# Performance work log

Hardware: AMD Instinct MI355X
Metric: run time of the kernel (lower is better)

## Reference

```python
import jax, jax.numpy as jnp
import numpy as np

N, F_IN, F_OUT = 8192, 512, 128
NEG_SLOPE = 0.2
MASK_VAL = -9e16


def setup_inputs() -> dict:
    key = jax.random.key(0)
    k_x, k_adj, k_w, k_a = jax.random.split(key, 4)
    x = jax.random.normal(k_x, (N, F_IN), dtype=jnp.float32)
    adj = jax.random.randint(k_adj, (N, N), 0, 2, dtype=jnp.int32)
    # xavier_normal_ init: std = sqrt(2 / (fan_in + fan_out))
    w = jax.random.normal(k_w, (F_IN, F_OUT), dtype=jnp.float32) * np.sqrt(2.0 / (F_IN + F_OUT))
    a = jax.random.normal(k_a, (2 * F_OUT, 1), dtype=jnp.float32) * np.sqrt(2.0 / (2 * F_OUT + 1))
    return {"x": x, "adj": adj, "w": w, "a": a}


def reference(x, adj, w, a):
    f_out = w.shape[1]
    h = x @ w                                   # [N, f_out]
    source_scores = h @ a[:f_out]               # [N, 1]
    target_scores = h @ a[f_out:]               # [N, 1]
    e = source_scores + target_scores.T         # [N, N] outer sum
    e = jax.nn.leaky_relu(e, negative_slope=NEG_SLOPE)
    e = jnp.where(adj > 0, e, jnp.float32(MASK_VAL))
    attention = jax.nn.softmax(e, axis=-1)      # [N, N]
    h_prime = attention @ h                     # [N, f_out]
    return attention, h_prime
```

## Files before the change

### kernel.cpp

```cpp
#include <hip/hip_runtime.h>
#include <hip/hip_bf16.h>

typedef unsigned short u16;
typedef unsigned int u32;
typedef __attribute__((ext_vector_type(8))) short short8;
typedef __attribute__((ext_vector_type(4))) float f32x4;

#define NN 8192
#define FIN 512
#define FOUT 128
#define NEG 0.2f
#define L2E 1.44269504088896340736f
#define EXP2(x) __builtin_amdgcn_exp2f(x)
#define LOG2(x) __builtin_amdgcn_logf(x)

__device__ __forceinline__ u16 f2bf(float f) {
  u32 u = __builtin_bit_cast(u32, f);
  u32 r = (u + 0x7fffu + ((u >> 16) & 1u)) >> 16;
  return (u16)r;
}

__global__ __launch_bounds__(256) void k_h(const float* __restrict__ x,
                                           const float* __restrict__ w,
                                           const float* __restrict__ av,
                                           u16* __restrict__ hb,
                                           float* __restrict__ sg,
                                           float* __restrict__ tgo) {
  __shared__ float xs[16][68];
  __shared__ float ws_[64][128];
  __shared__ u16 ht[16][130];
  const int t = threadIdx.x;
  const int r0 = blockIdx.x * 16;
  const int r = t >> 4;
  const int cq = (t & 15) * 4;
  float acc[2][4] = {};
  for (int kc = 0; kc < FIN; kc += 64) {
    __syncthreads();
    {
      const int rr = t >> 4, cc = (t & 15) * 4;
      *(float4*)&xs[rr][cc] = *(const float4*)(x + (size_t)(r0 + rr) * FIN + kc + cc);
    }
#pragma unroll
    for (int i = 0; i < 8; ++i) {
      const int off = i * 1024 + t * 4;
      const int wr = off >> 7, wc = off & 127;
      *(float4*)&ws_[wr][wc] = *(const float4*)(w + (size_t)(kc + wr) * FOUT + wc);
    }
    __syncthreads();
    for (int kk = 0; kk < 64; ++kk) {
      const float xv = xs[r][kk];
#pragma unroll
      for (int g = 0; g < 2; ++g) {
        const float4 wv = *(const float4*)&ws_[kk][cq + 64 * g];
        acc[g][0] = fmaf(xv, wv.x, acc[g][0]);
        acc[g][1] = fmaf(xv, wv.y, acc[g][1]);
        acc[g][2] = fmaf(xv, wv.z, acc[g][2]);
        acc[g][3] = fmaf(xv, wv.w, acc[g][3]);
      }
    }
  }
  const int rg = r0 + r;
  float sp = 0.f, tp = 0.f;
#pragma unroll
  for (int g = 0; g < 2; ++g) {
#pragma unroll
    for (int e = 0; e < 4; ++e) {
      const int n = cq + 64 * g + e;
      const float v = acc[g][e];
      ht[r][n] = f2bf(v);
      sp = fmaf(v, av[n], sp);
      tp = fmaf(v, av[FOUT + n], tp);
    }
  }
#pragma unroll
  for (int d = 1; d < 16; d <<= 1) {
    sp += __shfl_xor(sp, d);
    tp += __shfl_xor(tp, d);
  }
  if ((t & 15) == 0) { sg[rg] = sp; tgo[rg] = tp; }
  __syncthreads();
  {
    const int half = blockIdx.x & 1;
    u16* dst = hb + (size_t)(blockIdx.x >> 1) * 4096;
    union { short8 v; u16 us[8]; } b1;
    const int i1 = t * 8;
    const int o1 = (i1 >> 8) * 512 + half * 256 + (i1 & 255);
    const int nblk = i1 >> 8;
#pragma unroll
    for (int q = 0; q < 8; ++q) {
      const int j = (i1 + q) & 255;
      b1.us[q] = ht[((j >> 7) & 1) * 8 + (j & 7)][nblk * 16 + ((j >> 3) & 15)];
    }
    *(short8*)(dst + o1) = b1.v;
  }
}

__global__ __launch_bounds__(1024, 2) void k_maskA(const int* __restrict__ adj,
                                                   const float* __restrict__ sg,
                                                   const float* __restrict__ tg,
                                                   u32* __restrict__ maskR,
                                                   u32* __restrict__ maskT,
                                                   float* __restrict__ c2g) {
  __shared__ u32 mlds[16][257];
  const int tid = threadIdx.x;
  const int w = tid >> 6, lane = tid & 63;
  const int r0 = blockIdx.x << 4;
  const int row = r0 + w;
  const float sv = sg[row];
  const int4* ap = (const int4*)(adj + (size_t)row * NN);
  float sum = 0.f;
#pragma unroll 4
  for (int it = 0; it < 32; ++it) {
    const int4 a0 = ap[it * 64 + lane];
    const float4 tv = *(const float4*)(tg + it * 256 + lane * 4);
    u32 nib = 0u;
    float e, p, sm = 0.f;
    e = sv + tv.x; e = fmaxf(e, NEG * e); p = EXP2(e * L2E); sm += (a0.x > 0) ? p : 0.f; nib |= (a0.x > 0) ? 1u : 0u;
    e = sv + tv.y; e = fmaxf(e, NEG * e); p = EXP2(e * L2E); sm += (a0.y > 0) ? p : 0.f; nib |= (a0.y > 0) ? 2u : 0u;
    e = sv + tv.z; e = fmaxf(e, NEG * e); p = EXP2(e * L2E); sm += (a0.z > 0) ? p : 0.f; nib |= (a0.z > 0) ? 4u : 0u;
    e = sv + tv.w; e = fmaxf(e, NEG * e); p = EXP2(e * L2E); sm += (a0.w > 0) ? p : 0.f; nib |= (a0.w > 0) ? 8u : 0u;
    sum += sm;
    u32 v0 = nib;
    v0 |= __shfl_xor(v0, 1) << 4;
    v0 |= __shfl_xor(v0, 2) << 8;
    v0 |= __shfl_xor(v0, 4) << 16;
    if ((lane & 7) == 0) mlds[w][it * 8 + (lane >> 3)] = v0;
  }
#pragma unroll
  for (int d = 1; d < 64; d <<= 1) sum += __shfl_xor(sum, d);
  if (lane == 0) c2g[row] = -LOG2(sum);
  __syncthreads();
  for (int idx = tid; idx < 4096; idx += 1024) {
    const u32 v = mlds[idx >> 8][idx & 255];
    maskR[(size_t)(r0 + (idx >> 8)) * 256 + (idx & 255)] = v;
    maskT[(size_t)(idx & 255) * NN + r0 + (idx >> 8)] = v;
  }
}

__global__ __launch_bounds__(512, 4) void k_spv(const float* __restrict__ sg,
                                                const float* __restrict__ tg,
                                                const float* __restrict__ c2g,
                                                const u32* __restrict__ maskR,
                                                const u32* __restrict__ maskT,
                                                const u16* __restrict__ hb,
                                                float* __restrict__ att,
                                                float* __restrict__ part) {
  const int tid = threadIdx.x;
  const int w = tid >> 6, lane = tid & 63;
  if (blockIdx.x < 512) {
    const int mt = blockIdx.x >> 3, kt = blockIdx.x & 7;
    const int wr = w >> 1, ch = w & 1;
    const int wrow = mt * 128 + wr * 32;
    const int arow = lane & 15, kg = lane >> 4;
    const int rowA = wrow + arow, rowB = wrow + 16 + arow;
    const float sA = sg[rowA], cA = c2g[rowA];
    const float sB = sg[rowB], cB = c2g[rowB];
    f32x4 acc0[4], acc1[4];
#pragma unroll
    for (int j = 0; j < 4; ++j) {
      acc0[j] = (f32x4){0.f, 0.f, 0.f, 0.f};
      acc1[j] = (f32x4){0.f, 0.f, 0.f, 0.f};
    }
    const int kg8 = kg * 8;
#pragma unroll 2
    for (int step = 0; step < 32; ++step) {
      const int kgrp = kt * 32 + step;
      const int k0 = kgrp * 32;
      const u32 wdA = maskT[(size_t)kgrp * NN + rowA];
      const u32 wdB = maskT[(size_t)kgrp * NN + rowB];
      const u32 bA = (wdA >> kg8) & 0xffu;
      const u32 bB = (wdB >> kg8) & 0xffu;
      const float4 t0 = *(const float4*)(tg + k0 + kg8);
      const float4 t1 = *(const float4*)(tg + k0 + kg8 + 4);
      const float tv[8] = {t0.x, t0.y, t0.z, t0.w, t1.x, t1.y, t1.z, t1.w};
      union { short8 s8; u32 u[4]; } afA, afB;
      {
        float p[8];
#pragma unroll
        for (int e = 0; e < 8; ++e) {
          float ev = sA + tv[e];
          ev = fmaxf(ev, NEG * ev);
          p[e] = ((bA >> e) & 1u) ? EXP2(fmaf(ev, L2E, cA)) : 0.f;
        }
#pragma unroll
        for (int h2 = 0; h2 < 4; ++h2)
          afA.u[h2] = (u32)f2bf(p[2 * h2]) | ((u32)f2bf(p[2 * h2 + 1]) << 16);
      }
      {
        float p[8];
#pragma unroll
        for (int e = 0; e < 8; ++e) {
          float ev = sB + tv[e];
          ev = fmaxf(ev, NEG * ev);
          p[e] = ((bB >> e) & 1u) ? EXP2(fmaf(ev, L2E, cB)) : 0.f;
        }
#pragma unroll
        for (int h2 = 0; h2 < 4; ++h2)
          afB.u[h2] = (u32)f2bf(p[2 * h2]) | ((u32)f2bf(p[2 * h2 + 1]) << 16);
      }
      const u16* base = hb + (size_t)kgrp * 4096 + ch * 2048 + lane * 8;
#pragma unroll
      for (int j = 0; j < 4; ++j) {
        const short8 bf = *(const short8*)(base + j * 512);
        acc0[j] = __builtin_amdgcn_mfma_f32_16x16x32_bf16(afA.s8, bf, acc0[j], 0, 0, 0);
        acc1[j] = __builtin_amdgcn_mfma_f32_16x16x32_bf16(afB.s8, bf, acc1[j], 0, 0, 0);
      }
    }
    float* pslice = part + (size_t)kt * (NN * FOUT);
#pragma unroll
    for (int j = 0; j < 4; ++j) {
      const int col = (ch * 4 + j) * 16 + arow;
#pragma unroll
      for (int q = 0; q < 4; ++q) {
        pslice[(size_t)(wrow + kg * 4 + q) * FOUT + col] = acc0[j][q];
        pslice[(size_t)(wrow + 16 + kg * 4 + q) * FOUT + col] = acc1[j][q];
      }
    }
  } else {
    const int sb = blockIdx.x - 512;
    const int row = sb * 4 + (w >> 1);
    const int half = w & 1;
    const float sv = sg[row];
    const float c2 = c2g[row];
    const u32* mrow = maskR + (size_t)row * 256 + half * 128;
    const float* tbase = tg + half * 4096;
    float* abase = att + (size_t)row * NN + half * 4096;
    const u32 sh = (lane & 7) * 4;
#pragma unroll 4
    for (int it = 0; it < 16; ++it) {
      const int jo = it * 256 + lane * 4;
      const u32 wd = mrow[it * 8 + (lane >> 3)];
      const u32 nib = (wd >> sh) & 0xfu;
      const float4 tv = *(const float4*)(tbase + jo);
      float e0 = sv + tv.x; e0 = fmaxf(e0, NEG * e0);
      float e1 = sv + tv.y; e1 = fmaxf(e1, NEG * e1);
      float e2 = sv + tv.z; e2 = fmaxf(e2, NEG * e2);
      float e3 = sv + tv.w; e3 = fmaxf(e3, NEG * e3);
      f32x4 o;
      o.x = (nib & 1u) ? EXP2(fmaf(e0, L2E, c2)) : 0.f;
      o.y = (nib & 2u) ? EXP2(fmaf(e1, L2E, c2)) : 0.f;
      o.z = (nib & 4u) ? EXP2(fmaf(e2, L2E, c2)) : 0.f;
      o.w = (nib & 8u) ? EXP2(fmaf(e3, L2E, c2)) : 0.f;
      __builtin_nontemporal_store(o, (f32x4*)(abase + jo));
    }
  }
}

__global__ __launch_bounds__(256) void k_red(const float* __restrict__ part,
                                             float* __restrict__ hp) {
  const int i = (blockIdx.x * 256 + threadIdx.x) * 4;
  f32x4 s = (f32x4){0.f, 0.f, 0.f, 0.f};
#pragma unroll
  for (int kt = 0; kt < 8; ++kt)
    s += *(const f32x4*)(part + (size_t)kt * (NN * FOUT) + i);
  *(f32x4*)(hp + i) = s;
}

extern "C" void kernel_launch(void* const* d_in, const int* in_sizes, int n_in,
                              void* d_out, int out_size, void* d_ws, size_t ws_size,
                              hipStream_t stream) {
  const float* x = (const float*)d_in[0];
  const int* adj = (const int*)d_in[1];
  const float* w = (const float*)d_in[2];
  const float* a = (const float*)d_in[3];
  float* out = (float*)d_out;
  float* att = out;
  float* hp = out + (size_t)NN * NN;
  u16* hb = (u16*)d_ws;
  float* s = (float*)((char*)d_ws + (size_t)2 * 1024 * 1024);
  float* t = s + NN;
  float* c2 = t + NN;
  u32* maskR = (u32*)((char*)d_ws + (size_t)4 * 1024 * 1024);
  u32* maskT = (u32*)((char*)d_ws + (size_t)12 * 1024 * 1024);
  float* part = (float*)((char*)d_ws + (size_t)20 * 1024 * 1024);

  k_h<<<512, 256, 0, stream>>>(x, w, a, hb, s, t);
  k_maskA<<<512, 1024, 0, stream>>>(adj, s, t, maskR, maskT, c2);
  k_spv<<<2560, 512, 0, stream>>>(s, t, c2, maskR, maskT, hb, att, part);
  k_red<<<1024, 256, 0, stream>>>(part, hp);
}
```

Measured before the change: 188.5 us.

## Fuse attention-row write into mask pass; split PV matmul into own kernel

The mask/row-sum kernel now keeps each row's mask bits in registers and writes the normalized attention row immediately after computing the log-sum. This removes the row-major mask buffer and the separate attention-writing blocks in the combined kernel. The transposed mask is written directly to global memory without an LDS staging step, and adj is read with nontemporal loads. The PV matmul becomes its own smaller launch. In exchange, the exponentials are recomputed in the same kernel, which lengthens it, and the transposed-mask stores become scattered 4-byte writes.

```diff
diff --git a/kernel.cpp b/kernel.cpp
--- a/kernel.cpp
+++ b/kernel.cpp
@@ -5,6 +5,7 @@
 typedef unsigned int u32;
 typedef __attribute__((ext_vector_type(8))) short short8;
 typedef __attribute__((ext_vector_type(4))) float f32x4;
+typedef __attribute__((ext_vector_type(4))) int i32x4;
 
 #define NN 8192
 #define FIN 512
@@ -95,23 +96,21 @@
   }
 }
 
-__global__ __launch_bounds__(1024, 2) void k_maskA(const int* __restrict__ adj,
-                                                   const float* __restrict__ sg,
-                                                   const float* __restrict__ tg,
-                                                   u32* __restrict__ maskR,
-                                                   u32* __restrict__ maskT,
-                                                   float* __restrict__ c2g) {
-  __shared__ u32 mlds[16][257];
-  const int tid = threadIdx.x;
-  const int w = tid >> 6, lane = tid & 63;
-  const int r0 = blockIdx.x << 4;
-  const int row = r0 + w;
+__global__ __launch_bounds__(512, 2) void k_fms(const int* __restrict__ adj,
+                                                const float* __restrict__ sg,
+                                                const float* __restrict__ tg,
+                                                u32* __restrict__ maskT,
+                                                float* __restrict__ c2g,
+                                                float* __restrict__ att) {
+  const int w = threadIdx.x >> 6, lane = threadIdx.x & 63;
+  const int row = blockIdx.x * 8 + w;
   const float sv = sg[row];
-  const int4* ap = (const int4*)(adj + (size_t)row * NN);
+  const i32x4* ap = (const i32x4*)(adj + (size_t)row * NN);
+  u32 bank[4] = {0u, 0u, 0u, 0u};
   float sum = 0.f;
-#pragma unroll 4
+#pragma unroll
   for (int it = 0; it < 32; ++it) {
-    const int4 a0 = ap[it * 64 + lane];
+    const i32x4 a0 = __builtin_nontemporal_load(ap + it * 64 + lane);
     const float4 tv = *(const float4*)(tg + it * 256 + lane * 4);
     u32 nib = 0u;
     float e, p, sm = 0.f;
@@ -120,128 +119,110 @@
     e = sv + tv.z; e = fmaxf(e, NEG * e); p = EXP2(e * L2E); sm += (a0.z > 0) ? p : 0.f; nib |= (a0.z > 0) ? 4u : 0u;
     e = sv + tv.w; e = fmaxf(e, NEG * e); p = EXP2(e * L2E); sm += (a0.w > 0) ? p : 0.f; nib |= (a0.w > 0) ? 8u : 0u;
     sum += sm;
+    bank[it >> 3] |= nib << ((it & 7) * 4);
     u32 v0 = nib;
     v0 |= __shfl_xor(v0, 1) << 4;
     v0 |= __shfl_xor(v0, 2) << 8;
     v0 |= __shfl_xor(v0, 4) << 16;
-    if ((lane & 7) == 0) mlds[w][it * 8 + (lane >> 3)] = v0;
+    if ((lane & 7) == 0)
+      maskT[(size_t)(it * 8 + (lane >> 3)) * NN + row] = v0;
   }
 #pragma unroll
   for (int d = 1; d < 64; d <<= 1) sum += __shfl_xor(sum, d);
-  if (lane == 0) c2g[row] = -LOG2(sum);
-  __syncthreads();
-  for (int idx = tid; idx < 4096; idx += 1024) {
-    const u32 v = mlds[idx >> 8][idx & 255];
-    maskR[(size_t)(r0 + (idx >> 8)) * 256 + (idx & 255)] = v;
-    maskT[(size_t)(idx & 255) * NN + r0 + (idx >> 8)] = v;
-  }
-}
-
-__global__ __launch_bounds__(512, 4) void k_spv(const float* __restrict__ sg,
-                                                const float* __restrict__ tg,
-                                                const float* __restrict__ c2g,
-                                                const u32* __restrict__ maskR,
-                                                const u32* __restrict__ maskT,
-                                                const u16* __restrict__ hb,
-                                                float* __restrict__ att,
-                                                float* __restrict__ part) {
+  const float c2 = -LOG2(sum);
+  if (lane == 0) c2g[row] = c2;
+  float* abase = att + (size_t)row * NN;
+#pragma unroll
+  for (int it = 0; it < 32; ++it) {
+    const u32 nib = (bank[it >> 3] >> ((it & 7) * 4)) & 0xfu;
+    const float4 tv = *(const float4*)(tg + it * 256 + lane * 4);
+    float e0 = sv + tv.x; e0 = fmaxf(e0, NEG * e0);
+    float e1 = sv + tv.y; e1 = fmaxf(e1, NEG * e1);
+    float e2 = sv + tv.z; e2 = fmaxf(e2, NEG * e2);
+    float e3 = sv + tv.w; e3 = fmaxf(e3, NEG * e3);
+    f32x4 o;
+    o.x = (nib & 1u) ? EXP2(fmaf(e0, L2E, c2)) : 0.f;
+    o.y = (nib & 2u) ? EXP2(fmaf(e1, L2E, c2)) : 0.f;
+    o.z = (nib & 4u) ? EXP2(fmaf(e2, L2E, c2)) : 0.f;
+    o.w = (nib & 8u) ? EXP2(fmaf(e3, L2E, c2)) : 0.f;
+    __builtin_nontemporal_store(o, (f32x4*)(abase + it * 256 + lane * 4));
+  }
+}
+
+__global__ __launch_bounds__(512, 2) void k_pv(const float* __restrict__ sg,
+                                               const float* __restrict__ tg,
+                                               const float* __restrict__ c2g,
+                                               const u32* __restrict__ maskT,
+                                               const u16* __restrict__ hb,
+                                               float* __restrict__ part) {
   const int tid = threadIdx.x;
   const int w = tid >> 6, lane = tid & 63;
-  if (blockIdx.x < 512) {
-    const int mt = blockIdx.x >> 3, kt = blockIdx.x & 7;
-    const int wr = w >> 1, ch = w & 1;
-    const int wrow = mt * 128 + wr * 32;
-    const int arow = lane & 15, kg = lane >> 4;
-    const int rowA = wrow + arow, rowB = wrow + 16 + arow;
-    const float sA = sg[rowA], cA = c2g[rowA];
-    const float sB = sg[rowB], cB = c2g[rowB];
-    f32x4 acc0[4], acc1[4];
+  const int mt = blockIdx.x >> 3, kt = blockIdx.x & 7;
+  const int wr = w >> 1, ch = w & 1;
+  const int wrow = mt * 128 + wr * 32;
+  const int arow = lane & 15, kg = lane >> 4;
+  const int rowA = wrow + arow, rowB = wrow + 16 + arow;
+  const float sA = sg[rowA], cA = c2g[rowA];
+  const float sB = sg[rowB], cB = c2g[rowB];
+  f32x4 acc0[4], acc1[4];
+#pragma unroll
+  for (int j = 0; j < 4; ++j) {
+    acc0[j] = (f32x4){0.f, 0.f, 0.f, 0.f};
+    acc1[j] = (f32x4){0.f, 0.f, 0.f, 0.f};
+  }
+  const int kg8 = kg * 8;
+#pragma unroll 2
+  for (int step = 0; step < 32; ++step) {
+    const int kgrp = kt * 32 + step;
+    const int k0 = kgrp * 32;
+    const u32 wdA = maskT[(size_t)kgrp * NN + rowA];
+    const u32 wdB = maskT[(size_t)kgrp * NN + rowB];
+    const u32 bA = (wdA >> kg8) & 0xffu;
+    const u32 bB = (wdB >> kg8) & 0xffu;
+    const float4 t0 = *(const float4*)(tg + k0 + kg8);
+    const float4 t1 = *(const float4*)(tg + k0 + kg8 + 4);
+    const float tv[8] = {t0.x, t0.y, t0.z, t0.w, t1.x, t1.y, t1.z, t1.w};
+    union { short8 s8; u32 u[4]; } afA, afB;
+    {
+      float p[8];
+#pragma unroll
+      for (int e = 0; e < 8; ++e) {
+        float ev = sA + tv[e];
+        ev = fmaxf(ev, NEG * ev);
+        p[e] = ((bA >> e) & 1u) ? EXP2(fmaf(ev, L2E, cA)) : 0.f;
+      }
+#pragma unroll
+      for (int h2 = 0; h2 < 4; ++h2)
+        afA.u[h2] = (u32)f2bf(p[2 * h2]) | ((u32)f2bf(p[2 * h2 + 1]) << 16);
+    }
+    {
+      float p[8];
+#pragma unroll
+      for (int e = 0; e < 8; ++e) {
+        float ev = sB + tv[e];
+        ev = fmaxf(ev, NEG * ev);
+        p[e] = ((bB >> e) & 1u) ? EXP2(fmaf(ev, L2E, cB)) : 0.f;
+      }
+#pragma unroll
+      for (int h2 = 0; h2 < 4; ++h2)
+        afB.u[h2] = (u32)f2bf(p[2 * h2]) | ((u32)f2bf(p[2 * h2 + 1]) << 16);
+    }
+    const u16* base = hb + (size_t)kgrp * 4096 + ch * 2048 + lane * 8;
 #pragma unroll
     for (int j = 0; j < 4; ++j) {
-      acc0[j] = (f32x4){0.f, 0.f, 0.f, 0.f};
-      acc1[j] = (f32x4){0.f, 0.f, 0.f, 0.f};
-    }
-    const int kg8 = kg * 8;
-#pragma unroll 2
-    for (int step = 0; step < 32; ++step) {
-      const int kgrp = kt * 32 + step;
-      const int k0 = kgrp * 32;
-      const u32 wdA = maskT[(size_t)kgrp * NN + rowA];
-      const u32 wdB = maskT[(size_t)kgrp * NN + rowB];
-      const u32 bA = (wdA >> kg8) & 0xffu;
-      const u32 bB = (wdB >> kg8) & 0xffu;
-      const float4 t0 = *(const float4*)(tg + k0 + kg8);
-      const float4 t1 = *(const float4*)(tg + k0 + kg8 + 4);
-      const float tv[8] = {t0.x, t0.y, t0.z, t0.w, t1.x, t1.y, t1.z, t1.w};
-      union { short8 s8; u32 u[4]; } afA, afB;
-      {
-        float p[8];
-#pragma unroll
-        for (int e = 0; e < 8; ++e) {
-          float ev = sA + tv[e];
-          ev = fmaxf(ev, NEG * ev);
-          p[e] = ((bA >> e) & 1u) ? EXP2(fmaf(ev, L2E, cA)) : 0.f;
-        }
-#pragma unroll
-        for (int h2 = 0; h2 < 4; ++h2)
-          afA.u[h2] = (u32)f2bf(p[2 * h2]) | ((u32)f2bf(p[2 * h2 + 1]) << 16);
-      }
-      {
-        float p[8];
-#pragma unroll
-        for (int e = 0; e < 8; ++e) {
-          float ev = sB + tv[e];
-          ev = fmaxf(ev, NEG * ev);
-          p[e] = ((bB >> e) & 1u) ? EXP2(fmaf(ev, L2E, cB)) : 0.f;
-        }
-#pragma unroll
-        for (int h2 = 0; h2 < 4; ++h2)
-          afB.u[h2] = (u32)f2bf(p[2 * h2]) | ((u32)f2bf(p[2 * h2 + 1]) << 16);
-      }
-      const u16* base = hb + (size_t)kgrp * 4096 + ch * 2048 + lane * 8;
-#pragma unroll
-      for (int j = 0; j < 4; ++j) {
-        const short8 bf = *(const short8*)(base + j * 512);
-        acc0[j] = __builtin_amdgcn_mfma_f32_16x16x32_bf16(afA.s8, bf, acc0[j], 0, 0, 0);
-        acc1[j] = __builtin_amdgcn_mfma_f32_16x16x32_bf16(afB.s8, bf, acc1[j], 0, 0, 0);
-      }
-    }
-    float* pslice = part + (size_t)kt * (NN * FOUT);
-#pragma unroll
-    for (int j = 0; j < 4; ++j) {
-      const int col = (ch * 4 + j) * 16 + arow;
-#pragma unroll
-      for (int q = 0; q < 4; ++q) {
-        pslice[(size_t)(wrow + kg * 4 + q) * FOUT + col] = acc0[j][q];
-        pslice[(size_t)(wrow + 16 + kg * 4 + q) * FOUT + col] = acc1[j][q];
-      }
-    }
-  } else {
-    const int sb = blockIdx.x - 512;
-    const int row = sb * 4 + (w >> 1);
-    const int half = w & 1;
-    const float sv = sg[row];
-    const float c2 = c2g[row];
-    const u32* mrow = maskR + (size_t)row * 256 + half * 128;
-    const float* tbase = tg + half * 4096;
-    float* abase = att + (size_t)row * NN + half * 4096;
-    const u32 sh = (lane & 7) * 4;
-#pragma unroll 4
-    for (int it = 0; it < 16; ++it) {
-      const int jo = it * 256 + lane * 4;
-      const u32 wd = mrow[it * 8 + (lane >> 3)];
-      const u32 nib = (wd >> sh) & 0xfu;
-      const float4 tv = *(const float4*)(tbase + jo);
-      float e0 = sv + tv.x; e0 = fmaxf(e0, NEG * e0);
-      float e1 = sv + tv.y; e1 = fmaxf(e1, NEG * e1);
-      float e2 = sv + tv.z; e2 = fmaxf(e2, NEG * e2);
-      float e3 = sv + tv.w; e3 = fmaxf(e3, NEG * e3);
-      f32x4 o;
-      o.x = (nib & 1u) ? EXP2(fmaf(e0, L2E, c2)) : 0.f;
-      o.y = (nib & 2u) ? EXP2(fmaf(e1, L2E, c2)) : 0.f;
-      o.z = (nib & 4u) ? EXP2(fmaf(e2, L2E, c2)) : 0.f;
-      o.w = (nib & 8u) ? EXP2(fmaf(e3, L2E, c2)) : 0.f;
-      __builtin_nontemporal_store(o, (f32x4*)(abase + jo));
+      const short8 bf = *(const short8*)(base + j * 512);
+      acc0[j] = __builtin_amdgcn_mfma_f32_16x16x32_bf16(afA.s8, bf, acc0[j], 0, 0, 0);
+      acc1[j] = __builtin_amdgcn_mfma_f32_16x16x32_bf16(afB.s8, bf, acc1[j], 0, 0, 0);
+    }
+  }
+  float* pslice = part + (size_t)kt * (NN * FOUT);
+#pragma unroll
+  for (int j = 0; j < 4; ++j) {
+    const int col = (ch * 4 + j) * 16 + arow;
+#pragma unroll
+    for (int q = 0; q < 4; ++q) {
+      pslice[(size_t)(wrow + kg * 4 + q) * FOUT + col] = acc0[j][q];
+      pslice[(size_t)(wrow + 16 + kg * 4 + q) * FOUT + col] = acc1[j][q];
     }
   }
 }
@@ -270,12 +251,11 @@
   float* s = (float*)((char*)d_ws + (size_t)2 * 1024 * 1024);
   float* t = s + NN;
   float* c2 = t + NN;
-  u32* maskR = (u32*)((char*)d_ws + (size_t)4 * 1024 * 1024);
-  u32* maskT = (u32*)((char*)d_ws + (size_t)12 * 1024 * 1024);
-  float* part = (float*)((char*)d_ws + (size_t)20 * 1024 * 1024);
+  u32* maskT = (u32*)((char*)d_ws + (size_t)4 * 1024 * 1024);
+  float* part = (float*)((char*)d_ws + (size_t)12 * 1024 * 1024);
 
   k_h<<<512, 256, 0, stream>>>(x, w, a, hb, s, t);
-  k_maskA<<<512, 1024, 0, stream>>>(adj, s, t, maskR, maskT, c2);
-  k_spv<<<2560, 512, 0, stream>>>(s, t, c2, maskR, maskT, hb, att, part);
+  k_fms<<<1024, 512, 0, stream>>>(adj, s, t, maskT, c2, att);
+  k_pv<<<512, 512, 0, stream>>>(s, t, c2, maskT, hb, part);
   k_red<<<1024, 256, 0, stream>>>(part, hp);
 }
```

Measured after the change: 225.7 us. 19.8% more time.

## Process two adjacency rows per wave in mask kernel with nontemporal loads

Applied to the files above, without the earlier changes.

The adjacency mask/row-sum kernel now handles 32 rows per block (two rows per wave), sharing the target-score load across both rows and halving the grid. Adjacency reads use nontemporal loads to avoid polluting cache with the 256 MB streaming input. The mask write-back loop is reordered so that consecutive threads write consecutive rows of the transposed mask (more coalesced maskT stores). The cost is more registers per thread and fewer blocks, which may reduce occupancy and latency hiding.

```diff
diff --git a/kernel.cpp b/kernel.cpp
--- a/kernel.cpp
+++ b/kernel.cpp
@@ -5,6 +5,7 @@
 typedef unsigned int u32;
 typedef __attribute__((ext_vector_type(8))) short short8;
 typedef __attribute__((ext_vector_type(4))) float f32x4;
+typedef __attribute__((ext_vector_type(4))) int i32x4;
 
 #define NN 8192
 #define FIN 512
@@ -101,39 +102,65 @@
                                                    u32* __restrict__ maskR,
                                                    u32* __restrict__ maskT,
                                                    float* __restrict__ c2g) {
-  __shared__ u32 mlds[16][257];
+  __shared__ u32 mlds[32][257];
   const int tid = threadIdx.x;
   const int w = tid >> 6, lane = tid & 63;
-  const int r0 = blockIdx.x << 4;
-  const int row = r0 + w;
-  const float sv = sg[row];
-  const int4* ap = (const int4*)(adj + (size_t)row * NN);
-  float sum = 0.f;
-#pragma unroll 4
+  const int r0 = blockIdx.x << 5;
+  const int rA = r0 + 2 * w, rB = rA + 1;
+  const float sA = sg[rA], sB = sg[rB];
+  const i32x4* apA = (const i32x4*)(adj + (size_t)rA * NN);
+  const i32x4* apB = (const i32x4*)(adj + (size_t)rB * NN);
+  float sumA = 0.f, sumB = 0.f;
+#pragma unroll 2
   for (int it = 0; it < 32; ++it) {
-    const int4 a0 = ap[it * 64 + lane];
+    const i32x4 a0 = __builtin_nontemporal_load(apA + it * 64 + lane);
+    const i32x4 a1 = __builtin_nontemporal_load(apB + it * 64 + lane);
     const float4 tv = *(const float4*)(tg + it * 256 + lane * 4);
-    u32 nib = 0u;
-    float e, p, sm = 0.f;
-    e = sv + tv.x; e = fmaxf(e, NEG * e); p = EXP2(e * L2E); sm += (a0.x > 0) ? p : 0.f; nib |= (a0.x > 0) ? 1u : 0u;
-    e = sv + tv.y; e = fmaxf(e, NEG * e); p = EXP2(e * L2E); sm += (a0.y > 0) ? p : 0.f; nib |= (a0.y > 0) ? 2u : 0u;
-    e = sv + tv.z; e = fmaxf(e, NEG * e); p = EXP2(e * L2E); sm += (a0.z > 0) ? p : 0.f; nib |= (a0.z > 0) ? 4u : 0u;
-    e = sv + tv.w; e = fmaxf(e, NEG * e); p = EXP2(e * L2E); sm += (a0.w > 0) ? p : 0.f; nib |= (a0.w > 0) ? 8u : 0u;
-    sum += sm;
-    u32 v0 = nib;
+    u32 nib0 = 0u, nib1 = 0u;
+    {
+      float e, p, sm = 0.f;
+      e = sA + tv.x; e = fmaxf(e, NEG * e); p = EXP2(e * L2E); sm += (a0.x > 0) ? p : 0.f; nib0 |= (a0.x > 0) ? 1u : 0u;
+      e = sA + tv.y; e = fmaxf(e, NEG * e); p = EXP2(e * L2E); sm += (a0.y > 0) ? p : 0.f; nib0 |= (a0.y > 0) ? 2u : 0u;
+      e = sA + tv.z; e = fmaxf(e, NEG * e); p = EXP2(e * L2E); sm += (a0.z > 0) ? p : 0.f; nib0 |= (a0.z > 0) ? 4u : 0u;
+      e = sA + tv.w; e = fmaxf(e, NEG * e); p = EXP2(e * L2E); sm += (a0.w > 0) ? p : 0.f; nib0 |= (a0.w > 0) ? 8u : 0u;
+      sumA += sm;
+    }
+    {
+      float e, p, sm = 0.f;
+      e = sB + tv.x; e = fmaxf(e, NEG * e); p = EXP2(e * L2E); sm += (a1.x > 0) ? p : 0.f; nib1 |= (a1.x > 0) ? 1u : 0u;
+      e = sB + tv.y; e = fmaxf(e, NEG * e); p = EXP2(e * L2E); sm += (a1.y > 0) ? p : 0.f; nib1 |= (a1.y > 0) ? 2u : 0u;
+      e = sB + tv.z; e = fmaxf(e, NEG * e); p = EXP2(e * L2E); sm += (a1.z > 0) ? p : 0.f; nib1 |= (a1.z > 0) ? 4u : 0u;
+      e = sB + tv.w; e = fmaxf(e, NEG * e); p = EXP2(e * L2E); sm += (a1.w > 0) ? p : 0.f; nib1 |= (a1.w > 0) ? 8u : 0u;
+      sumB += sm;
+    }
+    u32 v0 = nib0;
     v0 |= __shfl_xor(v0, 1) << 4;
     v0 |= __shfl_xor(v0, 2) << 8;
     v0 |= __shfl_xor(v0, 4) << 16;
-    if ((lane & 7) == 0) mlds[w][it * 8 + (lane >> 3)] = v0;
-  }
-#pragma unroll
-  for (int d = 1; d < 64; d <<= 1) sum += __shfl_xor(sum, d);
-  if (lane == 0) c2g[row] = -LOG2(sum);
+    u32 v1 = nib1;
+    v1 |= __shfl_xor(v1, 1) << 4;
+    v1 |= __shfl_xor(v1, 2) << 8;
+    v1 |= __shfl_xor(v1, 4) << 16;
+    if ((lane & 7) == 0) {
+      mlds[2 * w][it * 8 + (lane >> 3)] = v0;
+      mlds[2 * w + 1][it * 8 + (lane >> 3)] = v1;
+    }
+  }
+#pragma unroll
+  for (int d = 1; d < 64; d <<= 1) {
+    sumA += __shfl_xor(sumA, d);
+    sumB += __shfl_xor(sumB, d);
+  }
+  if (lane == 0) {
+    c2g[rA] = -LOG2(sumA);
+    c2g[rB] = -LOG2(sumB);
+  }
   __syncthreads();
-  for (int idx = tid; idx < 4096; idx += 1024) {
-    const u32 v = mlds[idx >> 8][idx & 255];
-    maskR[(size_t)(r0 + (idx >> 8)) * 256 + (idx & 255)] = v;
-    maskT[(size_t)(idx & 255) * NN + r0 + (idx >> 8)] = v;
+  for (int idx = tid; idx < 8192; idx += 1024) {
+    const int wi = idx >> 5, rr = idx & 31;
+    const u32 v = mlds[rr][wi];
+    maskR[(size_t)(r0 + rr) * 256 + wi] = v;
+    maskT[(size_t)wi * NN + r0 + rr] = v;
   }
 }
 
@@ -275,7 +302,7 @@
   float* part = (float*)((char*)d_ws + (size_t)20 * 1024 * 1024);
 
   k_h<<<512, 256, 0, stream>>>(x, w, a, hb, s, t);
-  k_maskA<<<512, 1024, 0, stream>>>(adj, s, t, maskR, maskT, c2);
+  k_maskA<<<256, 1024, 0, stream>>>(adj, s, t, maskR, maskT, c2);
   k_spv<<<2560, 512, 0, stream>>>(s, t, c2, maskR, maskT, hb, att, part);
   k_red<<<1024, 256, 0, stream>>>(part, hp);
 }
```

Result: faster. 173.0 us (median of 2 runs) (-8.2%).
